# Optimization experiments

Measured on AMD Instinct MI355X. Metric: run time of the kernel, lower is better.

The kernel has to match this reference:

```python
import math
import jax, jax.numpy as jnp
import numpy as np

# ---- module hyperparameters (from init_kwargs) ----
N_DELTA, N_THETA, N_GAMMA = 32, 64, 256
N_TOTAL = N_DELTA + N_THETA + N_GAMMA  # 352
N_DIMS = 1024
BATCH = 4096
N_STEPS = 32
DT = 0.01
COUPLING = 2.0
PAC = 0.3
EPS = 1e-6
TWO_PI = 2.0 * math.pi


def setup_inputs() -> dict:
    key = jax.random.key(0)
    k0, k1, k2 = jax.random.split(key, 3)
    x = jax.random.normal(k0, (BATCH, N_DIMS), dtype=jnp.float32)
    # xavier_uniform with gain=0.5 for Linear(n_dims, n_total, bias=False)
    bound = 0.5 * math.sqrt(6.0 / (N_DIMS + N_TOTAL))
    W_phase = jax.random.uniform(k1, (N_TOTAL, N_DIMS), jnp.float32, -bound, bound)
    W_amp = jax.random.uniform(k2, (N_TOTAL, N_DIMS), jnp.float32, -bound, bound)
    # natural angular frequencies per band: delta ~2Hz, theta ~6Hz, gamma ~40Hz
    omega = jnp.concatenate([
        jnp.full((N_DELTA,), TWO_PI * 2.0, jnp.float32),
        jnp.full((N_THETA,), TWO_PI * 6.0, jnp.float32),
        jnp.full((N_GAMMA,), TWO_PI * 40.0, jnp.float32),
    ])
    # block-diagonal intra-band Kuramoto coupling, K_ij = coupling_strength / n_band
    Kn = np.zeros((N_TOTAL, N_TOTAL), dtype=np.float32)
    o = 0
    for nb in (N_DELTA, N_THETA, N_GAMMA):
        Kn[o:o + nb, o:o + nb] = COUPLING / nb
        o += nb
    K = jnp.asarray(Kn)
    return {"x": x, "W_phase": W_phase, "W_amp": W_amp, "omega": omega, "K": K}


def reference(x, W_phase, W_amp, omega, K):
    # learned projections -> initial phase in [0, 2pi), amplitude clamped >= eps
    phase0 = (x @ W_phase.T) % TWO_PI                      # (B, n_total)
    amp0 = jnp.maximum(jnp.abs(x @ W_amp.T), EPS)          # (B, n_total)

    def step(carry, _):
        phase, amp = carry
        s, c = jnp.sin(phase), jnp.cos(phase)
        # sum_j K_ij sin(phi_j - phi_i) = cos(phi_i)*(K@sin)_i - sin(phi_i)*(K@cos)_i
        coup = c * (s @ K.T) - s * (c @ K.T)
        phase_n = (phase + DT * (omega + coup)) % TWO_PI
        d = phase_n[:, :N_DELTA]
        t = phase_n[:, N_DELTA:N_DELTA + N_THETA]
        mean_d = jnp.arctan2(jnp.sin(d).mean(-1), jnp.cos(d).mean(-1))  # (B,)
        mean_t = jnp.arctan2(jnp.sin(t).mean(-1), jnp.cos(t).mean(-1))  # (B,)
        B = phase.shape[0]
        mod = jnp.concatenate([
            jnp.zeros((B, N_DELTA), phase.dtype),
            jnp.broadcast_to((PAC * jnp.cos(mean_d))[:, None], (B, N_THETA)),
            jnp.broadcast_to((PAC * jnp.cos(mean_t))[:, None], (B, N_GAMMA)),
        ], axis=-1)
        amp_n = jnp.maximum(amp * (1.0 + DT * mod), EPS)
        return (phase_n, amp_n), None

    (final_phase, final_amp), _ = jax.lax.scan(step, (phase0, amp0), None, length=N_STEPS)
    return final_amp
```

## Files before the change

kernel.cpp:

```cpp
#include <hip/hip_runtime.h>

typedef float  f32x4 __attribute__((ext_vector_type(4)));
typedef short  s16x8 __attribute__((ext_vector_type(8)));
typedef _Float16 h2 __attribute__((ext_vector_type(2)));
typedef unsigned short u16;
typedef u16 u16x4 __attribute__((ext_vector_type(4)));

#define N_DIMS 1024
#define N_OSC  352
#define BATCH  4096
#define EPSV   1e-6f
#define INV2PI 0.15915494309189535f

__device__ __forceinline__ u16 f2bf(float f){
  unsigned u = __builtin_bit_cast(unsigned, f);
  u += 0x7FFFu + ((u >> 16) & 1u);
  return (u16)(u >> 16);
}
__device__ __forceinline__ float bf2f(unsigned h){
  return __builtin_bit_cast(float, h << 16);
}

#define NX4 1048576
#define NW4 90112

__global__ __launch_bounds__(256) void convert_k(const f32x4* __restrict__ x,
    const f32x4* __restrict__ wp, const f32x4* __restrict__ wa,
    u16x4* __restrict__ xb, u16x4* __restrict__ wb){
  int i = blockIdx.x * 256 + threadIdx.x;
  f32x4 v; u16x4* dst;
  if (i < NX4) { v = x[i]; dst = xb + i; }
  else {
    int j = i - NX4;
    v = (j < NW4) ? wp[j] : wa[j - NW4];
    dst = wb + j;
  }
  u16x4 r;
  r[0]=f2bf(v[0]); r[1]=f2bf(v[1]); r[2]=f2bf(v[2]); r[3]=f2bf(v[3]);
  *dst = r;
}

__device__ __forceinline__ void gload16(const u16* g, u16* l){
  __builtin_amdgcn_global_load_lds(
      (const __attribute__((address_space(1))) unsigned int*)(g),
      (__attribute__((address_space(3))) unsigned int*)(l), 16, 0, 0);
}

__global__ __launch_bounds__(256) void gemm_k(const u16* __restrict__ xb,
    const u16* __restrict__ wb, u16* __restrict__ phase0, float* __restrict__ amp0){
  __shared__ u16 lds[2][8192];
  const int tid = threadIdx.x;
  const int l   = tid & 63;
  const int w   = tid >> 6;

  const int bid = blockIdx.x;
  const int xcd = bid & 7;
  const int r   = bid >> 3;
  const int mt  = xcd * 8 + r / 11;
  const int nt  = r % 11;
  const int m0  = mt * 64;
  const int n0  = nt * 64;

  const int srow = w*16 + (l >> 3);
  const int scol = (((l & 7) ^ (l >> 3)) * 8);
  const u16* ga = xb + (size_t)(m0 + srow) * N_DIMS + scol;
  const u16* gb = wb + (size_t)(n0 + srow) * N_DIMS + scol;

  #define STAGE(b, kt) { \
    const u16* gA = ga + (kt)*64; \
    const u16* gB = gb + (kt)*64; \
    gload16(gA,            &lds[b][w*1024]); \
    gload16(gA + 8*N_DIMS, &lds[b][w*1024 + 512]); \
    gload16(gB,            &lds[b][4096 + w*1024]); \
    gload16(gB + 8*N_DIMS, &lds[b][4096 + w*1024 + 512]); }

  const int rl = l & 15;
  const int q0 = l >> 4;
  const int sx = l & 7;
  const int wr = w >> 1, wc = w & 1;

  f32x4 acc[2][2] = {};
  STAGE(0, 0)
  __syncthreads();

  for (int kt = 0; kt < 16; kt++){
    const int cb = kt & 1;
    if (kt < 15) STAGE(cb^1, kt+1)
    s16x8 a[2][2], b[2][2];
    #pragma unroll
    for (int mi = 0; mi < 2; mi++)
    #pragma unroll
    for (int ks = 0; ks < 2; ks++){
      int off = (wr*32 + mi*16 + rl)*64 + (((ks*4 + q0) ^ sx) * 8);
      a[mi][ks] = *(const s16x8*)&lds[cb][off];
    }
    #pragma unroll
    for (int nj = 0; nj < 2; nj++)
    #pragma unroll
    for (int ks = 0; ks < 2; ks++){
      int off = 4096 + (wc*32 + nj*16 + rl)*64 + (((ks*4 + q0) ^ sx) * 8);
      b[nj][ks] = *(const s16x8*)&lds[cb][off];
    }
    #pragma unroll
    for (int ks = 0; ks < 2; ks++)
    #pragma unroll
    for (int mi = 0; mi < 2; mi++)
    #pragma unroll
    for (int nj = 0; nj < 2; nj++)
      acc[mi][nj] = __builtin_amdgcn_mfma_f32_16x16x32_bf16(a[mi][ks], b[nj][ks], acc[mi][nj], 0,0,0);
    __syncthreads();
  }
  #undef STAGE

  #pragma unroll
  for (int mi = 0; mi < 2; mi++)
  #pragma unroll
  for (int nj = 0; nj < 2; nj++){
    const int n = n0 + wc*32 + nj*16 + rl;
    #pragma unroll
    for (int rg = 0; rg < 4; rg++){
      const int m = m0 + wr*32 + mi*16 + q0*4 + rg;
      float v = acc[mi][nj][rg];
      if (n < N_OSC) { float t = v * INV2PI; t -= floorf(t); phase0[(size_t)m*N_OSC + n] = f2bf(t); }
      else           { amp0[(size_t)m*N_OSC + (n - N_OSC)] = fmaxf(fabsf(v), EPSV); }
    }
  }
}

__device__ __forceinline__ int ibc(h2 v){ return __builtin_bit_cast(int, v); }
__device__ __forceinline__ h2  hbc(int v){ return __builtin_bit_cast(h2, v); }

__device__ __forceinline__ h2 rowsum16(h2 x){
  int v = ibc(x);
  v = ibc(hbc(v) + hbc(__builtin_amdgcn_mov_dpp(v, 0x121, 0xF, 0xF, true)));
  v = ibc(hbc(v) + hbc(__builtin_amdgcn_mov_dpp(v, 0x122, 0xF, 0xF, true)));
  v = ibc(hbc(v) + hbc(__builtin_amdgcn_mov_dpp(v, 0x124, 0xF, 0xF, true)));
  v = ibc(hbc(v) + hbc(__builtin_amdgcn_mov_dpp(v, 0x128, 0xF, 0xF, true)));
  return hbc(v);
}

__device__ __forceinline__ void updp(h2& s, h2& c, h2 cA, h2 sA, h2 GS, h2 GC){
  h2 e  = c*GS - s*GC;
  h2 s1 = s*cA + c*sA;
  h2 c1 = c*cA - s*sA;
  s = s1 + c1*e;
  c = c1 - s1*e;
}

__device__ __forceinline__ h2 splat2(_Float16 v){ h2 r; r[0]=v; r[1]=v; return r; }

__global__ __launch_bounds__(256) void iter_k(const u16* __restrict__ phase0,
                                              float* __restrict__ amp){
  const int tid = threadIdx.x;
  const int l   = tid & 63;
  const int g   = l & 15;
  const int row = blockIdx.x*16 + (tid>>6)*4 + (l>>4);
  const size_t rb = (size_t)row * N_OSC;

  const h2 cAd = splat2((_Float16)0.99211470f), sAd = splat2((_Float16)0.12533323f);
  const h2 cAt = splat2((_Float16)0.92977649f), sAt = splat2((_Float16)0.36812455f);
  const h2 cAg = splat2((_Float16)-0.80901699f), sAg = splat2((_Float16)0.58778525f);
  const h2 kd = splat2((_Float16)6.25e-4f);
  const h2 kt = splat2((_Float16)3.125e-4f);
  const h2 kg = splat2((_Float16)7.8125e-5f);

  h2 sD, cD, sT[2], cT[2], sG[8], cG[8];
  {
    const u16* pr = phase0 + rb;
    unsigned dw = *(const unsigned*)(pr + 2*g);
    uint2 tw    = *(const uint2*)(pr + 32 + 4*g);
    uint4 g0w   = *(const uint4*)(pr + 96 + 16*g);
    uint4 g1w   = *(const uint4*)(pr + 96 + 16*g + 8);
    #define SC2(dS, dC, i, p0, p1) { \
      dS[i][0] = (_Float16)__builtin_amdgcn_sinf(p0); \
      dS[i][1] = (_Float16)__builtin_amdgcn_sinf(p1); \
      dC[i][0] = (_Float16)__builtin_amdgcn_cosf(p0); \
      dC[i][1] = (_Float16)__builtin_amdgcn_cosf(p1); }
    {
      float d0 = bf2f(dw & 0xFFFFu), d1 = bf2f(dw >> 16);
      sD[0] = (_Float16)__builtin_amdgcn_sinf(d0);
      sD[1] = (_Float16)__builtin_amdgcn_sinf(d1);
      cD[0] = (_Float16)__builtin_amdgcn_cosf(d0);
      cD[1] = (_Float16)__builtin_amdgcn_cosf(d1);
    }
    SC2(sT, cT, 0, bf2f(tw.x & 0xFFFFu), bf2f(tw.x >> 16))
    SC2(sT, cT, 1, bf2f(tw.y & 0xFFFFu), bf2f(tw.y >> 16))
    SC2(sG, cG, 0, bf2f(g0w.x & 0xFFFFu), bf2f(g0w.x >> 16))
    SC2(sG, cG, 1, bf2f(g0w.y & 0xFFFFu), bf2f(g0w.y >> 16))
    SC2(sG, cG, 2, bf2f(g0w.z & 0xFFFFu), bf2f(g0w.z >> 16))
    SC2(sG, cG, 3, bf2f(g0w.w & 0xFFFFu), bf2f(g0w.w >> 16))
    SC2(sG, cG, 4, bf2f(g1w.x & 0xFFFFu), bf2f(g1w.x >> 16))
    SC2(sG, cG, 5, bf2f(g1w.y & 0xFFFFu), bf2f(g1w.y >> 16))
    SC2(sG, cG, 6, bf2f(g1w.z & 0xFFFFu), bf2f(g1w.z >> 16))
    SC2(sG, cG, 7, bf2f(g1w.w & 0xFFFFu), bf2f(g1w.w >> 16))
    #undef SC2
  }

  h2 PD, PT, PG;
  #define REDUCE { \
    h2 pd; pd[0] = sD[0]+sD[1]; pd[1] = cD[0]+cD[1]; \
    h2 ts = sT[0]+sT[1], tc = cT[0]+cT[1]; \
    h2 pt; pt[0] = ts[0]+ts[1]; pt[1] = tc[0]+tc[1]; \
    h2 gs = ((sG[0]+sG[1])+(sG[2]+sG[3]))+((sG[4]+sG[5])+(sG[6]+sG[7])); \
    h2 gc = ((cG[0]+cG[1])+(cG[2]+cG[3]))+((cG[4]+cG[5])+(cG[6]+cG[7])); \
    h2 pg; pg[0] = gs[0]+gs[1]; pg[1] = gc[0]+gc[1]; \
    PD = rowsum16(pd); PT = rowsum16(pt); PG = rowsum16(pg); }

  REDUCE

  float Pth = 1.f, Pga = 1.f, mPth = 1.f, mPga = 1.f;
  for (int t = 0; t < 32; t++){
    h2 gd = PD * kd, gt = PT * kt, gg = PG * kg;
    h2 GSd = splat2(gd[0]), GCd = splat2(gd[1]);
    h2 GSt = splat2(gt[0]), GCt = splat2(gt[1]);
    h2 GSg = splat2(gg[0]), GCg = splat2(gg[1]);
    updp(sD, cD, cAd, sAd, GSd, GCd);
    updp(sT[0], cT[0], cAt, sAt, GSt, GCt);
    updp(sT[1], cT[1], cAt, sAt, GSt, GCt);
    #pragma unroll
    for (int i = 0; i < 8; i++) updp(sG[i], cG[i], cAg, sAg, GSg, GCg);
    REDUCE
    float Sd = (float)PD[0], Cd = (float)PD[1];
    float St = (float)PT[0], Ct = (float)PT[1];
    float ft = 1.f + 0.003f * Cd * __builtin_amdgcn_rsqf(Cd*Cd + Sd*Sd);
    float fg = 1.f + 0.003f * Ct * __builtin_amdgcn_rsqf(Ct*Ct + St*St);
    Pth *= ft; mPth = fminf(mPth, Pth);
    Pga *= fg; mPga = fminf(mPga, Pga);
  }
  #undef REDUCE

  const float cth = EPSV * Pth / mPth;
  const float cga = EPSV * Pga / mPga;
  {
    float4 a = *(const float4*)(amp + rb + 32 + 4*g);
    a.x = fmaxf(a.x*Pth, cth); a.y = fmaxf(a.y*Pth, cth);
    a.z = fmaxf(a.z*Pth, cth); a.w = fmaxf(a.w*Pth, cth);
    *(float4*)(amp + rb + 32 + 4*g) = a;
  }
  #pragma unroll
  for (int i = 0; i < 4; i++){
    float4 a = *(const float4*)(amp + rb + 96 + 16*g + 4*i);
    a.x = fmaxf(a.x*Pga, cga); a.y = fmaxf(a.y*Pga, cga);
    a.z = fmaxf(a.z*Pga, cga); a.w = fmaxf(a.w*Pga, cga);
    *(float4*)(amp + rb + 96 + 16*g + 4*i) = a;
  }
}

extern "C" void kernel_launch(void* const* d_in, const int* in_sizes, int n_in,
                              void* d_out, int out_size, void* d_ws, size_t ws_size,
                              hipStream_t stream){
  const float* x  = (const float*)d_in[0];
  const float* wp = (const float*)d_in[1];
  const float* wa = (const float*)d_in[2];
  float* out = (float*)d_out;
  char* ws = (char*)d_ws;
  u16* xb  = (u16*)(ws);
  u16* wb  = (u16*)(ws + 8388608);
  u16* phase0 = (u16*)(ws + 9830400);

  convert_k<<<4800, 256, 0, stream>>>((const f32x4*)x, (const f32x4*)wp, (const f32x4*)wa,
                                      (u16x4*)xb, (u16x4*)wb);
  gemm_k<<<704, 256, 0, stream>>>(xb, wb, phase0, out);
  iter_k<<<256, 256, 0, stream>>>(phase0, out);
}
```

Before: 32.14 us.

## Drop gamma-band phase projection and iteration since output never depends on it

```diff
diff --git a/kernel.cpp b/kernel.cpp
--- a/kernel.cpp
+++ b/kernel.cpp
@@ -8,6 +8,8 @@
 
 #define N_DIMS 1024
 #define N_OSC  352
+#define N_PH   96
+#define NTOT   448
 #define BATCH  4096
 #define EPSV   1e-6f
 #define INV2PI 0.15915494309189535f
@@ -22,17 +24,20 @@
 }
 
 #define NX4 1048576
-#define NW4 90112
+#define NWP4 24576
+#define NWA4 90112
+#define NCONV (NX4 + NWP4 + NWA4)
 
 __global__ __launch_bounds__(256) void convert_k(const f32x4* __restrict__ x,
     const f32x4* __restrict__ wp, const f32x4* __restrict__ wa,
     u16x4* __restrict__ xb, u16x4* __restrict__ wb){
   int i = blockIdx.x * 256 + threadIdx.x;
+  if (i >= NCONV) return;
   f32x4 v; u16x4* dst;
   if (i < NX4) { v = x[i]; dst = xb + i; }
   else {
     int j = i - NX4;
-    v = (j < NW4) ? wp[j] : wa[j - NW4];
+    v = (j < NWP4) ? wp[j] : wa[j - NWP4];
     dst = wb + j;
   }
   u16x4 r;
@@ -56,8 +61,8 @@
   const int bid = blockIdx.x;
   const int xcd = bid & 7;
   const int r   = bid >> 3;
-  const int mt  = xcd * 8 + r / 11;
-  const int nt  = r % 11;
+  const int mt  = xcd * 8 + r / 7;
+  const int nt  = r % 7;
   const int m0  = mt * 64;
   const int n0  = nt * 64;
 
@@ -121,8 +126,8 @@
     for (int rg = 0; rg < 4; rg++){
       const int m = m0 + wr*32 + mi*16 + q0*4 + rg;
       float v = acc[mi][nj][rg];
-      if (n < N_OSC) { float t = v * INV2PI; t -= floorf(t); phase0[(size_t)m*N_OSC + n] = f2bf(t); }
-      else           { amp0[(size_t)m*N_OSC + (n - N_OSC)] = fmaxf(fabsf(v), EPSV); }
+      if (n < N_PH) { float t = v * INV2PI; t -= floorf(t); phase0[(size_t)m*N_PH + n] = f2bf(t); }
+      else          { amp0[(size_t)m*N_OSC + (n - N_PH)] = fmaxf(fabsf(v), EPSV); }
     }
   }
 }
@@ -155,22 +160,19 @@
   const int l   = tid & 63;
   const int g   = l & 15;
   const int row = blockIdx.x*16 + (tid>>6)*4 + (l>>4);
-  const size_t rb = (size_t)row * N_OSC;
+  const size_t rb  = (size_t)row * N_OSC;
+  const size_t rbp = (size_t)row * N_PH;
 
   const h2 cAd = splat2((_Float16)0.99211470f), sAd = splat2((_Float16)0.12533323f);
   const h2 cAt = splat2((_Float16)0.92977649f), sAt = splat2((_Float16)0.36812455f);
-  const h2 cAg = splat2((_Float16)-0.80901699f), sAg = splat2((_Float16)0.58778525f);
   const h2 kd = splat2((_Float16)6.25e-4f);
   const h2 kt = splat2((_Float16)3.125e-4f);
-  const h2 kg = splat2((_Float16)7.8125e-5f);
-
-  h2 sD, cD, sT[2], cT[2], sG[8], cG[8];
+
+  h2 sD, cD, sT[2], cT[2];
   {
-    const u16* pr = phase0 + rb;
+    const u16* pr = phase0 + rbp;
     unsigned dw = *(const unsigned*)(pr + 2*g);
     uint2 tw    = *(const uint2*)(pr + 32 + 4*g);
-    uint4 g0w   = *(const uint4*)(pr + 96 + 16*g);
-    uint4 g1w   = *(const uint4*)(pr + 96 + 16*g + 8);
     #define SC2(dS, dC, i, p0, p1) { \
       dS[i][0] = (_Float16)__builtin_amdgcn_sinf(p0); \
       dS[i][1] = (_Float16)__builtin_amdgcn_sinf(p1); \
@@ -185,40 +187,26 @@
     }
     SC2(sT, cT, 0, bf2f(tw.x & 0xFFFFu), bf2f(tw.x >> 16))
     SC2(sT, cT, 1, bf2f(tw.y & 0xFFFFu), bf2f(tw.y >> 16))
-    SC2(sG, cG, 0, bf2f(g0w.x & 0xFFFFu), bf2f(g0w.x >> 16))
-    SC2(sG, cG, 1, bf2f(g0w.y & 0xFFFFu), bf2f(g0w.y >> 16))
-    SC2(sG, cG, 2, bf2f(g0w.z & 0xFFFFu), bf2f(g0w.z >> 16))
-    SC2(sG, cG, 3, bf2f(g0w.w & 0xFFFFu), bf2f(g0w.w >> 16))
-    SC2(sG, cG, 4, bf2f(g1w.x & 0xFFFFu), bf2f(g1w.x >> 16))
-    SC2(sG, cG, 5, bf2f(g1w.y & 0xFFFFu), bf2f(g1w.y >> 16))
-    SC2(sG, cG, 6, bf2f(g1w.z & 0xFFFFu), bf2f(g1w.z >> 16))
-    SC2(sG, cG, 7, bf2f(g1w.w & 0xFFFFu), bf2f(g1w.w >> 16))
     #undef SC2
   }
 
-  h2 PD, PT, PG;
+  h2 PD, PT;
   #define REDUCE { \
     h2 pd; pd[0] = sD[0]+sD[1]; pd[1] = cD[0]+cD[1]; \
     h2 ts = sT[0]+sT[1], tc = cT[0]+cT[1]; \
     h2 pt; pt[0] = ts[0]+ts[1]; pt[1] = tc[0]+tc[1]; \
-    h2 gs = ((sG[0]+sG[1])+(sG[2]+sG[3]))+((sG[4]+sG[5])+(sG[6]+sG[7])); \
-    h2 gc = ((cG[0]+cG[1])+(cG[2]+cG[3]))+((cG[4]+cG[5])+(cG[6]+cG[7])); \
-    h2 pg; pg[0] = gs[0]+gs[1]; pg[1] = gc[0]+gc[1]; \
-    PD = rowsum16(pd); PT = rowsum16(pt); PG = rowsum16(pg); }
+    PD = rowsum16(pd); PT = rowsum16(pt); }
 
   REDUCE
 
   float Pth = 1.f, Pga = 1.f, mPth = 1.f, mPga = 1.f;
   for (int t = 0; t < 32; t++){
-    h2 gd = PD * kd, gt = PT * kt, gg = PG * kg;
+    h2 gd = PD * kd, gt = PT * kt;
     h2 GSd = splat2(gd[0]), GCd = splat2(gd[1]);
     h2 GSt = splat2(gt[0]), GCt = splat2(gt[1]);
-    h2 GSg = splat2(gg[0]), GCg = splat2(gg[1]);
     updp(sD, cD, cAd, sAd, GSd, GCd);
     updp(sT[0], cT[0], cAt, sAt, GSt, GCt);
     updp(sT[1], cT[1], cAt, sAt, GSt, GCt);
-    #pragma unroll
-    for (int i = 0; i < 8; i++) updp(sG[i], cG[i], cAg, sAg, GSg, GCg);
     REDUCE
     float Sd = (float)PD[0], Cd = (float)PD[1];
     float St = (float)PT[0], Ct = (float)PT[1];
@@ -256,10 +244,10 @@
   char* ws = (char*)d_ws;
   u16* xb  = (u16*)(ws);
   u16* wb  = (u16*)(ws + 8388608);
-  u16* phase0 = (u16*)(ws + 9830400);
-
-  convert_k<<<4800, 256, 0, stream>>>((const f32x4*)x, (const f32x4*)wp, (const f32x4*)wa,
+  u16* phase0 = (u16*)(ws + 9306112);
+
+  convert_k<<<4544, 256, 0, stream>>>((const f32x4*)x, (const f32x4*)wp, (const f32x4*)wa,
                                       (u16x4*)xb, (u16x4*)wb);
-  gemm_k<<<704, 256, 0, stream>>>(xb, wb, phase0, out);
+  gemm_k<<<448, 256, 0, stream>>>(xb, wb, phase0, out);
   iter_k<<<256, 256, 0, stream>>>(phase0, out);
 }
```

New measurement: 31.54 us. About the same (-1.9%).
